# Kernel tuning notes

Hardware: AMD Instinct MI355X
Metric: run time of the kernel (lower is better)

Reference implementation:

```python
import jax, jax.numpy as jnp
import numpy as np

NUM_HEADS = 16


def rotary_pos_emb(x):
    # x: [b, h, s, d] with interleaved rotary pairs (d even)
    d, s = x.shape[-1], x.shape[-2]
    ts = jnp.arange(0, d, 2, dtype=jnp.float32)
    inv_freqs = 10000.0 ** (-ts / d)                      # [d/2]
    grid = jnp.arange(s, dtype=jnp.float32)[:, None] * inv_freqs[None, :]  # [s, d/2]
    sin = jnp.repeat(jnp.sin(grid), 2, axis=-1)           # [s, d]
    cos = jnp.repeat(jnp.cos(grid), 2, axis=-1)           # [s, d]
    x1, x2 = x[..., ::2], x[..., 1::2]
    xs = jnp.stack([-x2, x1], axis=-1).reshape(x.shape)   # rotate pairs
    return x * cos + xs * sin


def setup_inputs() -> dict:
    key = jax.random.key(0)
    ks = jax.random.split(key, 6)
    b, l, d = 2, 2048, 1024
    x = jax.random.normal(ks[0], (b, l, d), dtype=jnp.float32)
    # additive causal mask: 0 on/below diag, large negative above
    causal = jnp.tril(jnp.ones((l, l), dtype=bool))
    mask = jnp.where(causal, 0.0, -1e9).astype(jnp.float32)[None, None]  # [1,1,l,l]
    s = 0.01  # VarianceScaling(0.01)-ish small init
    Wq = jax.random.normal(ks[1], (d, d), dtype=jnp.float32) * s
    Wk = jax.random.normal(ks[2], (d, d), dtype=jnp.float32) * s
    Wv = jax.random.normal(ks[3], (d, d), dtype=jnp.float32) * s
    Wo = jax.random.normal(ks[4], (d, d), dtype=jnp.float32) * s
    return {"x": x, "mask": mask, "Wq": Wq, "Wk": Wk, "Wv": Wv, "Wo": Wo}


def reference(x, mask, Wq, Wk, Wv, Wo):
    b, l, d = x.shape
    h = NUM_HEADS
    k_sz = d // h
    split = lambda t: t.reshape(b, l, h, k_sz).transpose(0, 2, 1, 3)  # b h l k
    # NOTE: original scales q by 1/sqrt(model_dim) (not key_size), before RoPE
    q = split(x @ Wq / jnp.sqrt(jnp.float32(d)))
    q = rotary_pos_emb(q)
    k = rotary_pos_emb(split(x @ Wk))
    v = split(x @ Wv)
    logits = jnp.einsum('bhik,bhjk->bhij', q, k) + mask   # [b,h,l,l]
    a = jax.nn.softmax(logits, axis=-1)
    y = jnp.einsum('bhij,bhjv->bhiv', a, v)               # [b,h,l,k]
    y = y.transpose(0, 2, 1, 3).reshape(b, l, d)
    return y @ Wo
```

## Files before the change

kernel.cpp:

```cpp
#include <hip/hip_runtime.h>
#include <math.h>

#define L 2048
#define D 1024
#define H 16
#define KS 64
#define BBATCH 2

typedef float f32x4 __attribute__((ext_vector_type(4)));
typedef short s16x8 __attribute__((ext_vector_type(8)));

__device__ __forceinline__ ushort f2bf(float f) {
    union { float f; unsigned u; } v; v.f = f;
    unsigned lsb = (v.u >> 16) & 1u;
    v.u += 0x7fffu + lsb;
    return (ushort)(v.u >> 16);
}

__device__ __forceinline__ unsigned fbits(float f) {
    union { float f; unsigned u; } v; v.f = f; return v.u;
}

__device__ __forceinline__ void gl_lds16(const ushort* g, ushort* l) {
    __builtin_amdgcn_global_load_lds(
        (const __attribute__((address_space(1))) unsigned int*)g,
        (__attribute__((address_space(3))) unsigned int*)l, 16, 0, 0);
}

__global__ __launch_bounds__(256)
void conv_x(const float* __restrict__ x, ushort* __restrict__ xb)
{
    const int i = (blockIdx.x * 256 + threadIdx.x) * 4;
    const float4 v = *(const float4*)&x[i];
    ushort4 p = make_ushort4(f2bf(v.x), f2bf(v.y), f2bf(v.z), f2bf(v.w));
    *(ushort4*)&xb[i] = p;
}

__global__ __launch_bounds__(256)
void conv_w(const float* __restrict__ W0, const float* __restrict__ W1,
            const float* __restrict__ W2, const float* __restrict__ W3,
            ushort* __restrict__ Wt)
{
    const float* W = (blockIdx.z == 0) ? W0 : (blockIdx.z == 1) ? W1
                   : (blockIdx.z == 2) ? W2 : W3;
    ushort* out = Wt + (size_t)blockIdx.z * D * D;
    __shared__ float T[32][33];
    const int r0 = blockIdx.y * 32, c0 = blockIdx.x * 32;
    const int tr = threadIdx.x >> 3, tc = (threadIdx.x & 7) * 4;
    const float4 v = *(const float4*)&W[(size_t)(r0 + tr) * D + c0 + tc];
    T[tr][tc + 0] = v.x; T[tr][tc + 1] = v.y;
    T[tr][tc + 2] = v.z; T[tr][tc + 3] = v.w;
    __syncthreads();
    ushort4 p = make_ushort4(f2bf(T[tc + 0][tr]), f2bf(T[tc + 1][tr]),
                             f2bf(T[tc + 2][tr]), f2bf(T[tc + 3][tr]));
    *(ushort4*)&out[(size_t)(c0 + tr) * D + r0 + tc] = p;
}

__global__ __launch_bounds__(256)
void qkv_gemm(const ushort* __restrict__ A, const ushort* __restrict__ B,
              ushort* __restrict__ Qo, ushort* __restrict__ Ko,
              ushort* __restrict__ Vto)
{
    __shared__ __align__(16) ushort smem[18432];
    ushort* As = smem;
    ushort* Bs = smem + 4096;

    const int tid  = threadIdx.x;
    const int wv   = tid >> 6, lane = tid & 63;
    const int i16  = lane & 15, quad = lane >> 4;
    const int wr   = wv >> 1, wc = wv & 1;
    const int m0   = blockIdx.y * 128;
    const int n0   = blockIdx.x * 128;

    f32x4 acc[4][4];
    #pragma unroll
    for (int i = 0; i < 4; ++i)
        #pragma unroll
        for (int j = 0; j < 4; ++j) acc[i][j] = (f32x4){0.f, 0.f, 0.f, 0.f};

    for (int k0 = 0; k0 < D; k0 += 32) {
        __syncthreads();
        {
            int c = wv * 64 + lane;
            gl_lds16(A + (size_t)(m0 + (c >> 2)) * D + k0 + (c & 3) * 8,
                     As + (size_t)(wv * 64) * 8);
            c = 256 + wv * 64 + lane;
            gl_lds16(A + (size_t)(m0 + (c >> 2)) * D + k0 + (c & 3) * 8,
                     As + (size_t)(256 + wv * 64) * 8);
        }
        {
            int c = wv * 64 + lane;
            gl_lds16(B + (size_t)(n0 + (c >> 2)) * D + k0 + (c & 3) * 8,
                     Bs + (size_t)(wv * 64) * 8);
            c = 256 + wv * 64 + lane;
            gl_lds16(B + (size_t)(n0 + (c >> 2)) * D + k0 + (c & 3) * 8,
                     Bs + (size_t)(256 + wv * 64) * 8);
        }
        __syncthreads();
        s16x8 af[4], bf[4];
        #pragma unroll
        for (int mt = 0; mt < 4; ++mt)
            af[mt] = *(const s16x8*)&As[(wr * 64 + mt * 16 + i16) * 32 + quad * 8];
        #pragma unroll
        for (int nt = 0; nt < 4; ++nt)
            bf[nt] = *(const s16x8*)&Bs[(wc * 64 + nt * 16 + i16) * 32 + quad * 8];
        #pragma unroll
        for (int mt = 0; mt < 4; ++mt)
            #pragma unroll
            for (int nt = 0; nt < 4; ++nt)
                acc[mt][nt] = __builtin_amdgcn_mfma_f32_16x16x32_bf16(
                    af[mt], bf[nt], acc[mt][nt], 0, 0, 0);
    }

    if (m0 < 2048) {
        const bool isQ = (m0 < 1024);
        ushort* out = isQ ? Qo : Ko;
        const int mb = isQ ? m0 : (m0 - 1024);
        #pragma unroll
        for (int mt = 0; mt < 4; ++mt)
            #pragma unroll
            for (int nt = 0; nt < 4; ++nt) {
                const int token = n0 + wc * 64 + nt * 16 + i16;
                const int b = token >> 11, s = token & 2047;
                const int dim = mb + wr * 64 + mt * 16 + quad * 4;
                const int hh = dim >> 6, dd = dim & 63;
                const float sf = (float)s;
                ushort4 p;
                #pragma unroll
                for (int pr = 0; pr < 2; ++pr) {
                    float e = acc[mt][nt][2 * pr];
                    float o = acc[mt][nt][2 * pr + 1];
                    if (isQ) { e *= 0.03125f; o *= 0.03125f; }
                    const float inv = __expf(-(float)(dd + 2 * pr) *
                                             (9.210340371976184f / 64.0f));
                    const float ang = sf * inv;
                    float sn, cs;
                    sincosf(ang, &sn, &cs);
                    const float ne = e * cs - o * sn;
                    const float no = o * cs + e * sn;
                    if (pr == 0) { p.x = f2bf(ne); p.y = f2bf(no); }
                    else         { p.z = f2bf(ne); p.w = f2bf(no); }
                }
                *(ushort4*)&out[((size_t)(b * H + hh) * L + s) * KS + dd] = p;
            }
    } else {
        __syncthreads();
        ushort* T = smem + wv * 4608;
        const int vbase = (m0 - 2048) + wr * 64;
        const int tbase = n0 + wc * 64;
        #pragma unroll
        for (int mt = 0; mt < 4; ++mt)
            #pragma unroll
            for (int nt = 0; nt < 4; ++nt) {
                const int tl = nt * 16 + i16;
                #pragma unroll
                for (int r = 0; r < 4; ++r)
                    T[(mt * 16 + quad * 4 + r) * 72 + tl] = f2bf(acc[mt][nt][r]);
            }
        __builtin_amdgcn_s_waitcnt(0);
        const int tl0 = (lane & 7) * 8;
        #pragma unroll
        for (int c = 0; c < 8; ++c) {
            const int vl = c * 8 + (lane >> 3);
            const s16x8 val = *(const s16x8*)&T[vl * 72 + tl0];
            const int vdim = vbase + vl;
            const int hh = vdim >> 6, dd = vdim & 63;
            const int token0 = tbase + tl0;
            const int b = token0 >> 11, s0 = token0 & 2047;
            *(s16x8*)&Vto[((size_t)(b * H + hh) * KS + dd) * L + s0] = val;
        }
    }
}

__global__ __launch_bounds__(256)
void oproj_gemm(const ushort* __restrict__ A, const ushort* __restrict__ B,
                float* __restrict__ out)
{
    __shared__ __align__(16) ushort smem[8192];
    ushort* As = smem;
    ushort* Bs = smem + 4096;
    const int tid  = threadIdx.x;
    const int wv   = tid >> 6, lane = tid & 63;
    const int i16  = lane & 15, quad = lane >> 4;
    const int wr   = wv >> 1, wc = wv & 1;
    const int m0   = blockIdx.y * 128;
    const int n0   = blockIdx.x * 128;

    f32x4 acc[4][4];
    #pragma unroll
    for (int i = 0; i < 4; ++i)
        #pragma unroll
        for (int j = 0; j < 4; ++j) acc[i][j] = (f32x4){0.f, 0.f, 0.f, 0.f};

    for (int k0 = 0; k0 < D; k0 += 32) {
        __syncthreads();
        {
            int c = wv * 64 + lane;
            gl_lds16(A + (size_t)(m0 + (c >> 2)) * D + k0 + (c & 3) * 8,
                     As + (size_t)(wv * 64) * 8);
            c = 256 + wv * 64 + lane;
            gl_lds16(A + (size_t)(m0 + (c >> 2)) * D + k0 + (c & 3) * 8,
                     As + (size_t)(256 + wv * 64) * 8);
        }
        {
            int c = wv * 64 + lane;
            gl_lds16(B + (size_t)(n0 + (c >> 2)) * D + k0 + (c & 3) * 8,
                     Bs + (size_t)(wv * 64) * 8);
            c = 256 + wv * 64 + lane;
            gl_lds16(B + (size_t)(n0 + (c >> 2)) * D + k0 + (c & 3) * 8,
                     Bs + (size_t)(256 + wv * 64) * 8);
        }
        __syncthreads();
        s16x8 af[4], bf[4];
        #pragma unroll
        for (int mt = 0; mt < 4; ++mt)
            af[mt] = *(const s16x8*)&As[(wr * 64 + mt * 16 + i16) * 32 + quad * 8];
        #pragma unroll
        for (int nt = 0; nt < 4; ++nt)
            bf[nt] = *(const s16x8*)&Bs[(wc * 64 + nt * 16 + i16) * 32 + quad * 8];
        #pragma unroll
        for (int mt = 0; mt < 4; ++mt)
            #pragma unroll
            for (int nt = 0; nt < 4; ++nt)
                acc[mt][nt] = __builtin_amdgcn_mfma_f32_16x16x32_bf16(
                    af[mt], bf[nt], acc[mt][nt], 0, 0, 0);
    }

    #pragma unroll
    for (int mt = 0; mt < 4; ++mt)
        #pragma unroll
        for (int nt = 0; nt < 4; ++nt) {
            const int od = n0 + wc * 64 + nt * 16 + i16;
            const int tk = m0 + wr * 64 + mt * 16 + quad * 4;
            #pragma unroll
            for (int r = 0; r < 4; ++r)
                out[(size_t)(tk + r) * D + od] = acc[mt][nt][r];
        }
}

__global__ __launch_bounds__(512)
void attn_mfma(const ushort* __restrict__ Q, const ushort* __restrict__ K,
               const ushort* __restrict__ Vt, ushort* __restrict__ Yb)
{
    const int bh   = blockIdx.y;
    const int qa   = blockIdx.x;
    const int qb   = 31 - qa;
    const int tid  = threadIdx.x;
    const int wave = tid >> 6, lane = tid & 63;
    const int half = wave >> 2, wv4 = wave & 3;
    const int i16  = lane & 15, quad = lane >> 4;
    const int qt   = half ? qb : qa;
    const int r0   = qt * 64 + wv4 * 16;
    const int row  = r0 + i16;

    __shared__ ushort Ks[64 * 72];
    __shared__ ushort Vs[64 * 72];
    __shared__ ushort Ps[8][16 * 72];

    const ushort* Qb = Q  + (size_t)bh * L * KS;
    const ushort* Kb = K  + (size_t)bh * L * KS;
    const ushort* Vb = Vt + (size_t)bh * KS * L;

    const s16x8 qf0 = *(const s16x8*)(Qb + (size_t)row * KS + quad * 8);
    const s16x8 qf1 = *(const s16x8*)(Qb + (size_t)row * KS + 32 + quad * 8);

    const int sr = tid >> 3, sseg = (tid & 7) * 8;
    s16x8 kpre = *(const s16x8*)(Kb + (size_t)sr * KS + sseg);
    s16x8 vpre = *(const s16x8*)(Vb + (size_t)sr * L + sseg);
    *(s16x8*)&Ks[sr * 72 + sseg] = kpre;
    *(s16x8*)&Vs[sr * 72 + sseg] = vpre;
    __syncthreads();

    f32x4 O0 = {0.f,0.f,0.f,0.f}, O1 = O0, O2 = O0, O3 = O0;
    float psum = 0.0f;

    for (int jt = 0; jt <= qb; ++jt) {
        const int j0 = jt * 64;
        const bool has_next = (jt < qb);

        if (has_next) {
            const int j0n = j0 + 64;
            kpre = *(const s16x8*)(Kb + (size_t)(j0n + sr) * KS + sseg);
            vpre = *(const s16x8*)(Vb + (size_t)sr * L + j0n + sseg);
        }

        if (jt <= qt) {
            f32x4 st[4];
            #pragma unroll
            for (int nt = 0; nt < 4; ++nt) {
                const s16x8 kf0 = *(const s16x8*)&Ks[(nt * 16 + i16) * 72 + quad * 8];
                const s16x8 kf1 = *(const s16x8*)&Ks[(nt * 16 + i16) * 72 + 32 + quad * 8];
                f32x4 c = {0.f,0.f,0.f,0.f};
                c = __builtin_amdgcn_mfma_f32_16x16x32_bf16(kf0, qf0, c, 0, 0, 0);
                c = __builtin_amdgcn_mfma_f32_16x16x32_bf16(kf1, qf1, c, 0, 0, 0);
                st[nt] = c;
            }
            if (jt == qt) {
                #pragma unroll
                for (int nt = 0; nt < 4; ++nt)
                    #pragma unroll
                    for (int rg = 0; rg < 4; ++rg) {
                        const int j = j0 + nt * 16 + quad * 4 + rg;
                        if (j > row) st[nt][rg] = -1e30f;
                    }
            }
            float p[4][4];
            #pragma unroll
            for (int nt = 0; nt < 4; ++nt)
                #pragma unroll
                for (int rg = 0; rg < 4; ++rg) {
                    p[nt][rg] = __expf(st[nt][rg]);
                    psum += p[nt][rg];
                }
            ushort* P2 = &Ps[wave][0];
            #pragma unroll
            for (int nt = 0; nt < 4; ++nt) {
                uint2 pk;
                pk.x = __builtin_amdgcn_perm(fbits(p[nt][1]), fbits(p[nt][0]), 0x07060302u);
                pk.y = __builtin_amdgcn_perm(fbits(p[nt][3]), fbits(p[nt][2]), 0x07060302u);
                *(uint2*)(P2 + i16 * 72 + nt * 16 + quad * 4) = pk;
            }
            const s16x8 pf0 = *(const s16x8*)(P2 + i16 * 72 + quad * 8);
            const s16x8 pf1 = *(const s16x8*)(P2 + i16 * 72 + 32 + quad * 8);
            s16x8 v0, v1;
            v0 = *(const s16x8*)&Vs[(0 * 16 + i16) * 72 + quad * 8];
            v1 = *(const s16x8*)&Vs[(0 * 16 + i16) * 72 + 32 + quad * 8];
            O0 = __builtin_amdgcn_mfma_f32_16x16x32_bf16(v0, pf0, O0, 0, 0, 0);
            O0 = __builtin_amdgcn_mfma_f32_16x16x32_bf16(v1, pf1, O0, 0, 0, 0);
            v0 = *(const s16x8*)&Vs[(1 * 16 + i16) * 72 + quad * 8];
            v1 = *(const s16x8*)&Vs[(1 * 16 + i16) * 72 + 32 + quad * 8];
            O1 = __builtin_amdgcn_mfma_f32_16x16x32_bf16(v0, pf0, O1, 0, 0, 0);
            O1 = __builtin_amdgcn_mfma_f32_16x16x32_bf16(v1, pf1, O1, 0, 0, 0);
            v0 = *(const s16x8*)&Vs[(2 * 16 + i16) * 72 + quad * 8];
            v1 = *(const s16x8*)&Vs[(2 * 16 + i16) * 72 + 32 + quad * 8];
            O2 = __builtin_amdgcn_mfma_f32_16x16x32_bf16(v0, pf0, O2, 0, 0, 0);
            O2 = __builtin_amdgcn_mfma_f32_16x16x32_bf16(v1, pf1, O2, 0, 0, 0);
            v0 = *(const s16x8*)&Vs[(3 * 16 + i16) * 72 + quad * 8];
            v1 = *(const s16x8*)&Vs[(3 * 16 + i16) * 72 + 32 + quad * 8];
            O3 = __builtin_amdgcn_mfma_f32_16x16x32_bf16(v0, pf0, O3, 0, 0, 0);
            O3 = __builtin_amdgcn_mfma_f32_16x16x32_bf16(v1, pf1, O3, 0, 0, 0);
        }

        __syncthreads();
        if (has_next) {
            *(s16x8*)&Ks[sr * 72 + sseg] = kpre;
            *(s16x8*)&Vs[sr * 72 + sseg] = vpre;
        }
        __syncthreads();
    }

    psum += __shfl_xor(psum, 16);
    psum += __shfl_xor(psum, 32);
    const float inv_l = __builtin_amdgcn_rcpf(psum);
    const int b = bh >> 4, hh = bh & 15;
    ushort* Yp = Yb + ((size_t)(b * L + row)) * D + hh * KS + quad * 4;
    f32x4 r;
    r = O0 * inv_l; *(ushort4*)(Yp +  0) = make_ushort4(f2bf(r[0]),f2bf(r[1]),f2bf(r[2]),f2bf(r[3]));
    r = O1 * inv_l; *(ushort4*)(Yp + 16) = make_ushort4(f2bf(r[0]),f2bf(r[1]),f2bf(r[2]),f2bf(r[3]));
    r = O2 * inv_l; *(ushort4*)(Yp + 32) = make_ushort4(f2bf(r[0]),f2bf(r[1]),f2bf(r[2]),f2bf(r[3]));
    r = O3 * inv_l; *(ushort4*)(Yp + 48) = make_ushort4(f2bf(r[0]),f2bf(r[1]),f2bf(r[2]),f2bf(r[3]));
}

extern "C" void kernel_launch(void* const* d_in, const int* in_sizes, int n_in,
                              void* d_out, int out_size, void* d_ws, size_t ws_size,
                              hipStream_t stream)
{
    const float* x  = (const float*)d_in[0];
    const float* Wq = (const float*)d_in[2];
    const float* Wk = (const float*)d_in[3];
    const float* Wv = (const float*)d_in[4];
    const float* Wo = (const float*)d_in[5];

    const size_t NTOK = (size_t)BBATCH * L;
    const size_t SZ   = NTOK * D;
    ushort* xb  = (ushort*)d_ws;
    ushort* Wt  = xb + SZ;
    ushort* Qb  = Wt + 4 * (size_t)D * D;
    ushort* Kb  = Qb + SZ;
    ushort* Vtb = Kb + SZ;
    ushort* Yb  = Vtb + SZ;

    conv_x<<<dim3(SZ / 1024), dim3(256), 0, stream>>>(x, xb);
    conv_w<<<dim3(32, 32, 4), dim3(256), 0, stream>>>(Wq, Wk, Wv, Wo, Wt);

    qkv_gemm<<<dim3(32, 24), dim3(256), 0, stream>>>(Wt, xb, Qb, Kb, Vtb);

    attn_mfma<<<dim3(16, 32), dim3(512), 0, stream>>>(Qb, Kb, Vtb, Yb);

    oproj_gemm<<<dim3(8, 32), dim3(256), 0, stream>>>(Yb, Wt + 3 * (size_t)D * D,
                                                      (float*)d_out);
}
```

Measured before the change: 197.6 us.

## Fuse prep kernels, precompute RoPE table, split attention KV across waves, shrink oproj tiles

Merges the x and weight conversion kernels into one prep launch that also builds a cos/sin table for RoPE, which the QKV GEMM epilogue reads instead of calling sincosf per element. The attention kernel changes from pairing two query tiles per block to one query tile per block, with two wave groups each taking alternate KV tiles and merging partial outputs and sums through shared memory at the end. The output-projection GEMM uses 128x64 tiles for twice as many blocks. The cost is an extra table read and LDS reduction, and the table lives in the Yb buffer before attention overwrites it.

```diff
diff --git a/kernel.cpp b/kernel.cpp
--- a/kernel.cpp
+++ b/kernel.cpp
@@ -28,36 +28,47 @@
 }
 
 __global__ __launch_bounds__(256)
-void conv_x(const float* __restrict__ x, ushort* __restrict__ xb)
+void prep(const float* __restrict__ x,
+          const float* __restrict__ W0, const float* __restrict__ W1,
+          const float* __restrict__ W2, const float* __restrict__ W3,
+          ushort* __restrict__ xb, ushort* __restrict__ Wt,
+          float2* __restrict__ tab)
 {
-    const int i = (blockIdx.x * 256 + threadIdx.x) * 4;
-    const float4 v = *(const float4*)&x[i];
-    ushort4 p = make_ushort4(f2bf(v.x), f2bf(v.y), f2bf(v.z), f2bf(v.w));
-    *(ushort4*)&xb[i] = p;
-}
-
-__global__ __launch_bounds__(256)
-void conv_w(const float* __restrict__ W0, const float* __restrict__ W1,
-            const float* __restrict__ W2, const float* __restrict__ W3,
-            ushort* __restrict__ Wt)
-{
-    const float* W = (blockIdx.z == 0) ? W0 : (blockIdx.z == 1) ? W1
-                   : (blockIdx.z == 2) ? W2 : W3;
-    ushort* out = Wt + (size_t)blockIdx.z * D * D;
     __shared__ float T[32][33];
-    const int r0 = blockIdx.y * 32, c0 = blockIdx.x * 32;
-    const int tr = threadIdx.x >> 3, tc = (threadIdx.x & 7) * 4;
-    const float4 v = *(const float4*)&W[(size_t)(r0 + tr) * D + c0 + tc];
-    T[tr][tc + 0] = v.x; T[tr][tc + 1] = v.y;
-    T[tr][tc + 2] = v.z; T[tr][tc + 3] = v.w;
-    __syncthreads();
-    ushort4 p = make_ushort4(f2bf(T[tc + 0][tr]), f2bf(T[tc + 1][tr]),
-                             f2bf(T[tc + 2][tr]), f2bf(T[tc + 3][tr]));
-    *(ushort4*)&out[(size_t)(c0 + tr) * D + r0 + tc] = p;
+    const int bid = blockIdx.x;
+    const int tid = threadIdx.x;
+    if (bid < 4096) {
+        const int i = bid * 1024 + tid * 4;
+        const float4 v = *(const float4*)&x[i];
+        ushort4 p = make_ushort4(f2bf(v.x), f2bf(v.y), f2bf(v.z), f2bf(v.w));
+        *(ushort4*)&xb[i] = p;
+    } else if (bid < 8192) {
+        const int t = bid - 4096;
+        const int z = t >> 10;
+        const float* W = (z == 0) ? W0 : (z == 1) ? W1 : (z == 2) ? W2 : W3;
+        ushort* out = Wt + (size_t)z * D * D;
+        const int r0 = ((t >> 5) & 31) * 32, c0 = (t & 31) * 32;
+        const int tr = tid >> 3, tc = (tid & 7) * 4;
+        const float4 v = *(const float4*)&W[(size_t)(r0 + tr) * D + c0 + tc];
+        T[tr][tc + 0] = v.x; T[tr][tc + 1] = v.y;
+        T[tr][tc + 2] = v.z; T[tr][tc + 3] = v.w;
+        __syncthreads();
+        ushort4 p = make_ushort4(f2bf(T[tc + 0][tr]), f2bf(T[tc + 1][tr]),
+                                 f2bf(T[tc + 2][tr]), f2bf(T[tc + 3][tr]));
+        *(ushort4*)&out[(size_t)(c0 + tr) * D + r0 + tc] = p;
+    } else {
+        const int idx = (bid - 8192) * 256 + tid;
+        const int dd2 = idx >> 11, s = idx & 2047;
+        const float inv = __expf(-(float)(2 * dd2) * (9.210340371976184f / 64.0f));
+        float sn, cs;
+        sincosf((float)s * inv, &sn, &cs);
+        tab[idx] = make_float2(cs, sn);
+    }
 }
 
 __global__ __launch_bounds__(256)
 void qkv_gemm(const ushort* __restrict__ A, const ushort* __restrict__ B,
+              const float2* __restrict__ tab,
               ushort* __restrict__ Qo, ushort* __restrict__ Ko,
               ushort* __restrict__ Vto)
 {
@@ -124,20 +135,15 @@
                 const int b = token >> 11, s = token & 2047;
                 const int dim = mb + wr * 64 + mt * 16 + quad * 4;
                 const int hh = dim >> 6, dd = dim & 63;
-                const float sf = (float)s;
                 ushort4 p;
                 #pragma unroll
                 for (int pr = 0; pr < 2; ++pr) {
                     float e = acc[mt][nt][2 * pr];
                     float o = acc[mt][nt][2 * pr + 1];
                     if (isQ) { e *= 0.03125f; o *= 0.03125f; }
-                    const float inv = __expf(-(float)(dd + 2 * pr) *
-                                             (9.210340371976184f / 64.0f));
-                    const float ang = sf * inv;
-                    float sn, cs;
-                    sincosf(ang, &sn, &cs);
-                    const float ne = e * cs - o * sn;
-                    const float no = o * cs + e * sn;
+                    const float2 cssn = tab[(size_t)((dd >> 1) + pr) * 2048 + s];
+                    const float ne = e * cssn.x - o * cssn.y;
+                    const float no = o * cssn.x + e * cssn.y;
                     if (pr == 0) { p.x = f2bf(ne); p.y = f2bf(no); }
                     else         { p.z = f2bf(ne); p.w = f2bf(no); }
                 }
@@ -176,21 +182,20 @@
 void oproj_gemm(const ushort* __restrict__ A, const ushort* __restrict__ B,
                 float* __restrict__ out)
 {
-    __shared__ __align__(16) ushort smem[8192];
-    ushort* As = smem;
-    ushort* Bs = smem + 4096;
+    __shared__ __align__(16) ushort As[128 * 32];
+    __shared__ __align__(16) ushort Bs[64 * 32];
     const int tid  = threadIdx.x;
     const int wv   = tid >> 6, lane = tid & 63;
     const int i16  = lane & 15, quad = lane >> 4;
     const int wr   = wv >> 1, wc = wv & 1;
     const int m0   = blockIdx.y * 128;
-    const int n0   = blockIdx.x * 128;
-
-    f32x4 acc[4][4];
+    const int n0   = blockIdx.x * 64;
+
+    f32x4 acc[4][2];
     #pragma unroll
     for (int i = 0; i < 4; ++i)
         #pragma unroll
-        for (int j = 0; j < 4; ++j) acc[i][j] = (f32x4){0.f, 0.f, 0.f, 0.f};
+        for (int j = 0; j < 2; ++j) acc[i][j] = (f32x4){0.f, 0.f, 0.f, 0.f};
 
     for (int k0 = 0; k0 < D; k0 += 32) {
         __syncthreads();
@@ -206,22 +211,19 @@
             int c = wv * 64 + lane;
             gl_lds16(B + (size_t)(n0 + (c >> 2)) * D + k0 + (c & 3) * 8,
                      Bs + (size_t)(wv * 64) * 8);
-            c = 256 + wv * 64 + lane;
-            gl_lds16(B + (size_t)(n0 + (c >> 2)) * D + k0 + (c & 3) * 8,
-                     Bs + (size_t)(256 + wv * 64) * 8);
-        }
-        __syncthreads();
-        s16x8 af[4], bf[4];
+        }
+        __syncthreads();
+        s16x8 af[4], bf[2];
         #pragma unroll
         for (int mt = 0; mt < 4; ++mt)
             af[mt] = *(const s16x8*)&As[(wr * 64 + mt * 16 + i16) * 32 + quad * 8];
         #pragma unroll
-        for (int nt = 0; nt < 4; ++nt)
-            bf[nt] = *(const s16x8*)&Bs[(wc * 64 + nt * 16 + i16) * 32 + quad * 8];
-        #pragma unroll
-        for (int mt = 0; mt < 4; ++mt)
-            #pragma unroll
-            for (int nt = 0; nt < 4; ++nt)
+        for (int nt = 0; nt < 2; ++nt)
+            bf[nt] = *(const s16x8*)&Bs[(wc * 32 + nt * 16 + i16) * 32 + quad * 8];
+        #pragma unroll
+        for (int mt = 0; mt < 4; ++mt)
+            #pragma unroll
+            for (int nt = 0; nt < 2; ++nt)
                 acc[mt][nt] = __builtin_amdgcn_mfma_f32_16x16x32_bf16(
                     af[mt], bf[nt], acc[mt][nt], 0, 0, 0);
     }
@@ -229,8 +231,8 @@
     #pragma unroll
     for (int mt = 0; mt < 4; ++mt)
         #pragma unroll
-        for (int nt = 0; nt < 4; ++nt) {
-            const int od = n0 + wc * 64 + nt * 16 + i16;
+        for (int nt = 0; nt < 2; ++nt) {
+            const int od = n0 + wc * 32 + nt * 16 + i16;
             const int tk = m0 + wr * 64 + mt * 16 + quad * 4;
             #pragma unroll
             for (int r = 0; r < 4; ++r)
@@ -243,19 +245,15 @@
                const ushort* __restrict__ Vt, ushort* __restrict__ Yb)
 {
     const int bh   = blockIdx.y;
-    const int qa   = blockIdx.x;
-    const int qb   = 31 - qa;
+    const int qt   = 31 - blockIdx.x;
     const int tid  = threadIdx.x;
     const int wave = tid >> 6, lane = tid & 63;
-    const int half = wave >> 2, wv4 = wave & 3;
+    const int qs   = wave & 3, par = wave >> 2;
     const int i16  = lane & 15, quad = lane >> 4;
-    const int qt   = half ? qb : qa;
-    const int r0   = qt * 64 + wv4 * 16;
-    const int row  = r0 + i16;
-
-    __shared__ ushort Ks[64 * 72];
-    __shared__ ushort Vs[64 * 72];
-    __shared__ ushort Ps[8][16 * 72];
+    const int row  = qt * 64 + qs * 16 + i16;
+
+    __shared__ __align__(16) ushort KVs[4][64 * 72];
+    __shared__ __align__(16) ushort Ps[8][16 * 72];
 
     const ushort* Qb = Q  + (size_t)bh * L * KS;
     const ushort* Kb = K  + (size_t)bh * L * KS;
@@ -264,38 +262,57 @@
     const s16x8 qf0 = *(const s16x8*)(Qb + (size_t)row * KS + quad * 8);
     const s16x8 qf1 = *(const s16x8*)(Qb + (size_t)row * KS + 32 + quad * 8);
 
-    const int sr = tid >> 3, sseg = (tid & 7) * 8;
-    s16x8 kpre = *(const s16x8*)(Kb + (size_t)sr * KS + sseg);
-    s16x8 vpre = *(const s16x8*)(Vb + (size_t)sr * L + sseg);
-    *(s16x8*)&Ks[sr * 72 + sseg] = kpre;
-    *(s16x8*)&Vs[sr * 72 + sseg] = vpre;
+    const int sr = tid >> 3, ss = (tid & 7) * 8;
+
+    s16x8 kpA, vpA, kpB, vpB;
+    kpA = *(const s16x8*)(Kb + (size_t)sr * KS + ss);
+    vpA = *(const s16x8*)(Vb + (size_t)sr * L + ss);
+    if (qt >= 1) {
+        kpB = *(const s16x8*)(Kb + (size_t)(64 + sr) * KS + ss);
+        vpB = *(const s16x8*)(Vb + (size_t)sr * L + 64 + ss);
+    }
+    *(s16x8*)&KVs[0][sr * 72 + ss] = kpA;
+    *(s16x8*)&KVs[1][sr * 72 + ss] = vpA;
+    if (qt >= 1) {
+        *(s16x8*)&KVs[2][sr * 72 + ss] = kpB;
+        *(s16x8*)&KVs[3][sr * 72 + ss] = vpB;
+    }
     __syncthreads();
 
     f32x4 O0 = {0.f,0.f,0.f,0.f}, O1 = O0, O2 = O0, O3 = O0;
     float psum = 0.0f;
 
-    for (int jt = 0; jt <= qb; ++jt) {
-        const int j0 = jt * 64;
-        const bool has_next = (jt < qb);
-
-        if (has_next) {
-            const int j0n = j0 + 64;
-            kpre = *(const s16x8*)(Kb + (size_t)(j0n + sr) * KS + sseg);
-            vpre = *(const s16x8*)(Vb + (size_t)sr * L + j0n + sseg);
-        }
-
-        if (jt <= qt) {
+    const ushort* Ksb = &KVs[par * 2][0];
+    const ushort* Vsb = &KVs[par * 2 + 1][0];
+    ushort* P2 = &Ps[wave][0];
+
+    for (int p = 0; ; ++p) {
+        const int jme = 2 * p + par;
+        const bool pn = (2 * p + 2 <= qt);
+
+        if (pn) {
+            const int ja = (2 * p + 2) * 64;
+            kpA = *(const s16x8*)(Kb + (size_t)(ja + sr) * KS + ss);
+            vpA = *(const s16x8*)(Vb + (size_t)sr * L + ja + ss);
+            if (2 * p + 3 <= qt) {
+                kpB = *(const s16x8*)(Kb + (size_t)(ja + 64 + sr) * KS + ss);
+                vpB = *(const s16x8*)(Vb + (size_t)sr * L + ja + 64 + ss);
+            }
+        }
+
+        if (jme <= qt) {
+            const int j0 = jme * 64;
             f32x4 st[4];
             #pragma unroll
             for (int nt = 0; nt < 4; ++nt) {
-                const s16x8 kf0 = *(const s16x8*)&Ks[(nt * 16 + i16) * 72 + quad * 8];
-                const s16x8 kf1 = *(const s16x8*)&Ks[(nt * 16 + i16) * 72 + 32 + quad * 8];
+                const s16x8 kf0 = *(const s16x8*)&Ksb[(nt * 16 + i16) * 72 + quad * 8];
+                const s16x8 kf1 = *(const s16x8*)&Ksb[(nt * 16 + i16) * 72 + 32 + quad * 8];
                 f32x4 c = {0.f,0.f,0.f,0.f};
                 c = __builtin_amdgcn_mfma_f32_16x16x32_bf16(kf0, qf0, c, 0, 0, 0);
                 c = __builtin_amdgcn_mfma_f32_16x16x32_bf16(kf1, qf1, c, 0, 0, 0);
                 st[nt] = c;
             }
-            if (jt == qt) {
+            if (jme == qt) {
                 #pragma unroll
                 for (int nt = 0; nt < 4; ++nt)
                     #pragma unroll
@@ -304,61 +321,85 @@
                         if (j > row) st[nt][rg] = -1e30f;
                     }
             }
-            float p[4][4];
+            float pv[4][4];
             #pragma unroll
             for (int nt = 0; nt < 4; ++nt)
                 #pragma unroll
                 for (int rg = 0; rg < 4; ++rg) {
-                    p[nt][rg] = __expf(st[nt][rg]);
-                    psum += p[nt][rg];
+                    pv[nt][rg] = __expf(st[nt][rg]);
+                    psum += pv[nt][rg];
                 }
-            ushort* P2 = &Ps[wave][0];
             #pragma unroll
             for (int nt = 0; nt < 4; ++nt) {
                 uint2 pk;
-                pk.x = __builtin_amdgcn_perm(fbits(p[nt][1]), fbits(p[nt][0]), 0x07060302u);
-                pk.y = __builtin_amdgcn_perm(fbits(p[nt][3]), fbits(p[nt][2]), 0x07060302u);
+                pk.x = __builtin_amdgcn_perm(fbits(pv[nt][1]), fbits(pv[nt][0]), 0x07060302u);
+                pk.y = __builtin_amdgcn_perm(fbits(pv[nt][3]), fbits(pv[nt][2]), 0x07060302u);
                 *(uint2*)(P2 + i16 * 72 + nt * 16 + quad * 4) = pk;
             }
             const s16x8 pf0 = *(const s16x8*)(P2 + i16 * 72 + quad * 8);
             const s16x8 pf1 = *(const s16x8*)(P2 + i16 * 72 + 32 + quad * 8);
             s16x8 v0, v1;
-            v0 = *(const s16x8*)&Vs[(0 * 16 + i16) * 72 + quad * 8];
-            v1 = *(const s16x8*)&Vs[(0 * 16 + i16) * 72 + 32 + quad * 8];
+            v0 = *(const s16x8*)&Vsb[(0 * 16 + i16) * 72 + quad * 8];
+            v1 = *(const s16x8*)&Vsb[(0 * 16 + i16) * 72 + 32 + quad * 8];
             O0 = __builtin_amdgcn_mfma_f32_16x16x32_bf16(v0, pf0, O0, 0, 0, 0);
             O0 = __builtin_amdgcn_mfma_f32_16x16x32_bf16(v1, pf1, O0, 0, 0, 0);
-            v0 = *(const s16x8*)&Vs[(1 * 16 + i16) * 72 + quad * 8];
-            v1 = *(const s16x8*)&Vs[(1 * 16 + i16) * 72 + 32 + quad * 8];
+            v0 = *(const s16x8*)&Vsb[(1 * 16 + i16) * 72 + quad * 8];
+            v1 = *(const s16x8*)&Vsb[(1 * 16 + i16) * 72 + 32 + quad * 8];
             O1 = __builtin_amdgcn_mfma_f32_16x16x32_bf16(v0, pf0, O1, 0, 0, 0);
             O1 = __builtin_amdgcn_mfma_f32_16x16x32_bf16(v1, pf1, O1, 0, 0, 0);
-            v0 = *(const s16x8*)&Vs[(2 * 16 + i16) * 72 + quad * 8];
-            v1 = *(const s16x8*)&Vs[(2 * 16 + i16) * 72 + 32 + quad * 8];
+            v0 = *(const s16x8*)&Vsb[(2 * 16 + i16) * 72 + quad * 8];
+            v1 = *(const s16x8*)&Vsb[(2 * 16 + i16) * 72 + 32 + quad * 8];
             O2 = __builtin_amdgcn_mfma_f32_16x16x32_bf16(v0, pf0, O2, 0, 0, 0);
             O2 = __builtin_amdgcn_mfma_f32_16x16x32_bf16(v1, pf1, O2, 0, 0, 0);
-            v0 = *(const s16x8*)&Vs[(3 * 16 + i16) * 72 + quad * 8];
-            v1 = *(const s16x8*)&Vs[(3 * 16 + i16) * 72 + 32 + quad * 8];
+            v0 = *(const s16x8*)&Vsb[(3 * 16 + i16) * 72 + quad * 8];
+            v1 = *(const s16x8*)&Vsb[(3 * 16 + i16) * 72 + 32 + quad * 8];
             O3 = __builtin_amdgcn_mfma_f32_16x16x32_bf16(v0, pf0, O3, 0, 0, 0);
             O3 = __builtin_amdgcn_mfma_f32_16x16x32_bf16(v1, pf1, O3, 0, 0, 0);
         }
 
-        __syncthreads();
-        if (has_next) {
-            *(s16x8*)&Ks[sr * 72 + sseg] = kpre;
-            *(s16x8*)&Vs[sr * 72 + sseg] = vpre;
+        if (!pn) break;
+        __syncthreads();
+        {
+            *(s16x8*)&KVs[0][sr * 72 + ss] = kpA;
+            *(s16x8*)&KVs[1][sr * 72 + ss] = vpA;
+            if (2 * p + 3 <= qt) {
+                *(s16x8*)&KVs[2][sr * 72 + ss] = kpB;
+                *(s16x8*)&KVs[3][sr * 72 + ss] = vpB;
+            }
         }
         __syncthreads();
     }
 
     psum += __shfl_xor(psum, 16);
     psum += __shfl_xor(psum, 32);
-    const float inv_l = __builtin_amdgcn_rcpf(psum);
-    const int b = bh >> 4, hh = bh & 15;
-    ushort* Yp = Yb + ((size_t)(b * L + row)) * D + hh * KS + quad * 4;
-    f32x4 r;
-    r = O0 * inv_l; *(ushort4*)(Yp +  0) = make_ushort4(f2bf(r[0]),f2bf(r[1]),f2bf(r[2]),f2bf(r[3]));
-    r = O1 * inv_l; *(ushort4*)(Yp + 16) = make_ushort4(f2bf(r[0]),f2bf(r[1]),f2bf(r[2]),f2bf(r[3]));
-    r = O2 * inv_l; *(ushort4*)(Yp + 32) = make_ushort4(f2bf(r[0]),f2bf(r[1]),f2bf(r[2]),f2bf(r[3]));
-    r = O3 * inv_l; *(ushort4*)(Yp + 48) = make_ushort4(f2bf(r[0]),f2bf(r[1]),f2bf(r[2]),f2bf(r[3]));
+
+    __syncthreads();
+    float* Oex = (float*)&KVs[0][0];
+    float* Pex = Oex + 64 * 68;
+    const int obase = (qs * 16 + i16) * 68 + quad * 4;
+    if (par == 1) {
+        *(f32x4*)&Oex[obase +  0] = O0;
+        *(f32x4*)&Oex[obase + 16] = O1;
+        *(f32x4*)&Oex[obase + 32] = O2;
+        *(f32x4*)&Oex[obase + 48] = O3;
+        if (lane < 16) Pex[qs * 16 + i16] = psum;
+    }
+    __syncthreads();
+    if (par == 0) {
+        O0 += *(const f32x4*)&Oex[obase +  0];
+        O1 += *(const f32x4*)&Oex[obase + 16];
+        O2 += *(const f32x4*)&Oex[obase + 32];
+        O3 += *(const f32x4*)&Oex[obase + 48];
+        const float tot = psum + Pex[qs * 16 + i16];
+        const float inv_l = __builtin_amdgcn_rcpf(tot);
+        const int b = bh >> 4, hh = bh & 15;
+        ushort* Yp = Yb + ((size_t)(b * L + row)) * D + hh * KS + quad * 4;
+        f32x4 r;
+        r = O0 * inv_l; *(ushort4*)(Yp +  0) = make_ushort4(f2bf(r[0]),f2bf(r[1]),f2bf(r[2]),f2bf(r[3]));
+        r = O1 * inv_l; *(ushort4*)(Yp + 16) = make_ushort4(f2bf(r[0]),f2bf(r[1]),f2bf(r[2]),f2bf(r[3]));
+        r = O2 * inv_l; *(ushort4*)(Yp + 32) = make_ushort4(f2bf(r[0]),f2bf(r[1]),f2bf(r[2]),f2bf(r[3]));
+        r = O3 * inv_l; *(ushort4*)(Yp + 48) = make_ushort4(f2bf(r[0]),f2bf(r[1]),f2bf(r[2]),f2bf(r[3]));
+    }
 }
 
 extern "C" void kernel_launch(void* const* d_in, const int* in_sizes, int n_in,
@@ -379,14 +420,14 @@
     ushort* Kb  = Qb + SZ;
     ushort* Vtb = Kb + SZ;
     ushort* Yb  = Vtb + SZ;
-
-    conv_x<<<dim3(SZ / 1024), dim3(256), 0, stream>>>(x, xb);
-    conv_w<<<dim3(32, 32, 4), dim3(256), 0, stream>>>(Wq, Wk, Wv, Wo, Wt);
-
-    qkv_gemm<<<dim3(32, 24), dim3(256), 0, stream>>>(Wt, xb, Qb, Kb, Vtb);
-
-    attn_mfma<<<dim3(16, 32), dim3(512), 0, stream>>>(Qb, Kb, Vtb, Yb);
-
-    oproj_gemm<<<dim3(8, 32), dim3(256), 0, stream>>>(Yb, Wt + 3 * (size_t)D * D,
-                                                      (float*)d_out);
-}
+    float2* tab = (float2*)Yb;
+
+    prep<<<dim3(8448), dim3(256), 0, stream>>>(x, Wq, Wk, Wv, Wo, xb, Wt, tab);
+
+    qkv_gemm<<<dim3(32, 24), dim3(256), 0, stream>>>(Wt, xb, tab, Qb, Kb, Vtb);
+
+    attn_mfma<<<dim3(32, 32), dim3(512), 0, stream>>>(Qb, Kb, Vtb, Yb);
+
+    oproj_gemm<<<dim3(16, 32), dim3(256), 0, stream>>>(Yb, Wt + 3 * (size_t)D * D,
+                                                       (float*)d_out);
+}
```

After: 219.8 us. 11.2% more time.

## Merge prep kernels, tabulate RoPE sin/cos, stage Q/K stores via LDS, shrink oproj tile

Applied to the files above, without the earlier changes.

Fuses the x and weight bf16 conversion kernels into one prep launch, which also builds a precomputed cos/sin table for RoPE in the Y workspace buffer. The QKV GEMM epilogue reads that table instead of calling expf and sincosf per element, and stages rotated Q/K tiles in LDS so global stores become coalesced 16-byte rows. The output projection uses 128x64 tiles to double the block count for better CU occupancy. The table lookups add global reads, and reusing the Y buffer for the table relies on attention overwriting it afterwards.

```diff
diff --git a/kernel.cpp b/kernel.cpp
--- a/kernel.cpp
+++ b/kernel.cpp
@@ -28,36 +28,47 @@
 }
 
 __global__ __launch_bounds__(256)
-void conv_x(const float* __restrict__ x, ushort* __restrict__ xb)
+void prep(const float* __restrict__ x,
+          const float* __restrict__ W0, const float* __restrict__ W1,
+          const float* __restrict__ W2, const float* __restrict__ W3,
+          ushort* __restrict__ xb, ushort* __restrict__ Wt,
+          float2* __restrict__ tab)
 {
-    const int i = (blockIdx.x * 256 + threadIdx.x) * 4;
-    const float4 v = *(const float4*)&x[i];
-    ushort4 p = make_ushort4(f2bf(v.x), f2bf(v.y), f2bf(v.z), f2bf(v.w));
-    *(ushort4*)&xb[i] = p;
-}
-
-__global__ __launch_bounds__(256)
-void conv_w(const float* __restrict__ W0, const float* __restrict__ W1,
-            const float* __restrict__ W2, const float* __restrict__ W3,
-            ushort* __restrict__ Wt)
-{
-    const float* W = (blockIdx.z == 0) ? W0 : (blockIdx.z == 1) ? W1
-                   : (blockIdx.z == 2) ? W2 : W3;
-    ushort* out = Wt + (size_t)blockIdx.z * D * D;
     __shared__ float T[32][33];
-    const int r0 = blockIdx.y * 32, c0 = blockIdx.x * 32;
-    const int tr = threadIdx.x >> 3, tc = (threadIdx.x & 7) * 4;
-    const float4 v = *(const float4*)&W[(size_t)(r0 + tr) * D + c0 + tc];
-    T[tr][tc + 0] = v.x; T[tr][tc + 1] = v.y;
-    T[tr][tc + 2] = v.z; T[tr][tc + 3] = v.w;
-    __syncthreads();
-    ushort4 p = make_ushort4(f2bf(T[tc + 0][tr]), f2bf(T[tc + 1][tr]),
-                             f2bf(T[tc + 2][tr]), f2bf(T[tc + 3][tr]));
-    *(ushort4*)&out[(size_t)(c0 + tr) * D + r0 + tc] = p;
+    const int bid = blockIdx.x;
+    const int tid = threadIdx.x;
+    if (bid < 4096) {
+        const int i = bid * 1024 + tid * 4;
+        const float4 v = *(const float4*)&x[i];
+        ushort4 p = make_ushort4(f2bf(v.x), f2bf(v.y), f2bf(v.z), f2bf(v.w));
+        *(ushort4*)&xb[i] = p;
+    } else if (bid < 8192) {
+        const int t = bid - 4096;
+        const int z = t >> 10;
+        const float* W = (z == 0) ? W0 : (z == 1) ? W1 : (z == 2) ? W2 : W3;
+        ushort* out = Wt + (size_t)z * D * D;
+        const int r0 = ((t >> 5) & 31) * 32, c0 = (t & 31) * 32;
+        const int tr = tid >> 3, tc = (tid & 7) * 4;
+        const float4 v = *(const float4*)&W[(size_t)(r0 + tr) * D + c0 + tc];
+        T[tr][tc + 0] = v.x; T[tr][tc + 1] = v.y;
+        T[tr][tc + 2] = v.z; T[tr][tc + 3] = v.w;
+        __syncthreads();
+        ushort4 p = make_ushort4(f2bf(T[tc + 0][tr]), f2bf(T[tc + 1][tr]),
+                                 f2bf(T[tc + 2][tr]), f2bf(T[tc + 3][tr]));
+        *(ushort4*)&out[(size_t)(c0 + tr) * D + r0 + tc] = p;
+    } else {
+        const int idx = (bid - 8192) * 256 + tid;
+        const int dd2 = idx >> 11, s = idx & 2047;
+        const float inv = __expf(-(float)(2 * dd2) * (9.210340371976184f / 64.0f));
+        float sn, cs;
+        sincosf((float)s * inv, &sn, &cs);
+        tab[idx] = make_float2(cs, sn);
+    }
 }
 
 __global__ __launch_bounds__(256)
 void qkv_gemm(const ushort* __restrict__ A, const ushort* __restrict__ B,
+              const float2* __restrict__ tab,
               ushort* __restrict__ Qo, ushort* __restrict__ Ko,
               ushort* __restrict__ Vto)
 {
@@ -112,40 +123,48 @@
                     af[mt], bf[nt], acc[mt][nt], 0, 0, 0);
     }
 
+    __syncthreads();
+    ushort* T = smem + wv * 4608;
+
     if (m0 < 2048) {
         const bool isQ = (m0 < 1024);
         ushort* out = isQ ? Qo : Ko;
         const int mb = isQ ? m0 : (m0 - 1024);
-        #pragma unroll
-        for (int mt = 0; mt < 4; ++mt)
+        const int s0 = ((n0 + wc * 64) & 2047);
+        #pragma unroll
+        for (int mt = 0; mt < 4; ++mt) {
+            const int dd = mt * 16 + quad * 4;
             #pragma unroll
             for (int nt = 0; nt < 4; ++nt) {
-                const int token = n0 + wc * 64 + nt * 16 + i16;
-                const int b = token >> 11, s = token & 2047;
-                const int dim = mb + wr * 64 + mt * 16 + quad * 4;
-                const int hh = dim >> 6, dd = dim & 63;
-                const float sf = (float)s;
+                const int lt = nt * 16 + i16;
+                const int s = s0 + lt;
                 ushort4 p;
                 #pragma unroll
                 for (int pr = 0; pr < 2; ++pr) {
                     float e = acc[mt][nt][2 * pr];
                     float o = acc[mt][nt][2 * pr + 1];
                     if (isQ) { e *= 0.03125f; o *= 0.03125f; }
-                    const float inv = __expf(-(float)(dd + 2 * pr) *
-                                             (9.210340371976184f / 64.0f));
-                    const float ang = sf * inv;
-                    float sn, cs;
-                    sincosf(ang, &sn, &cs);
-                    const float ne = e * cs - o * sn;
-                    const float no = o * cs + e * sn;
+                    const float2 cssn = tab[(size_t)((dd >> 1) + pr) * 2048 + s];
+                    const float ne = e * cssn.x - o * cssn.y;
+                    const float no = o * cssn.x + e * cssn.y;
                     if (pr == 0) { p.x = f2bf(ne); p.y = f2bf(no); }
                     else         { p.z = f2bf(ne); p.w = f2bf(no); }
                 }
-                *(ushort4*)&out[((size_t)(b * H + hh) * L + s) * KS + dd] = p;
+                *(ushort4*)&T[lt * 72 + dd] = p;
             }
+        }
+        __builtin_amdgcn_s_waitcnt(0);
+        const int hh = (mb + wr * 64) >> 6;
+        const int tok0 = n0 + wc * 64;
+        const int b = tok0 >> 11;
+        const int dl = (lane & 7) * 8;
+        #pragma unroll
+        for (int c = 0; c < 8; ++c) {
+            const int tl = c * 8 + (lane >> 3);
+            const s16x8 val = *(const s16x8*)&T[tl * 72 + dl];
+            *(s16x8*)&out[((size_t)(b * H + hh) * L + (s0 + tl)) * KS + dl] = val;
+        }
     } else {
-        __syncthreads();
-        ushort* T = smem + wv * 4608;
         const int vbase = (m0 - 2048) + wr * 64;
         const int tbase = n0 + wc * 64;
         #pragma unroll
@@ -166,8 +185,8 @@
             const int vdim = vbase + vl;
             const int hh = vdim >> 6, dd = vdim & 63;
             const int token0 = tbase + tl0;
-            const int b = token0 >> 11, s0 = token0 & 2047;
-            *(s16x8*)&Vto[((size_t)(b * H + hh) * KS + dd) * L + s0] = val;
+            const int b = token0 >> 11, sv = token0 & 2047;
+            *(s16x8*)&Vto[((size_t)(b * H + hh) * KS + dd) * L + sv] = val;
         }
     }
 }
@@ -176,21 +195,20 @@
 void oproj_gemm(const ushort* __restrict__ A, const ushort* __restrict__ B,
                 float* __restrict__ out)
 {
-    __shared__ __align__(16) ushort smem[8192];
-    ushort* As = smem;
-    ushort* Bs = smem + 4096;
+    __shared__ __align__(16) ushort As[128 * 32];
+    __shared__ __align__(16) ushort Bs[64 * 32];
     const int tid  = threadIdx.x;
     const int wv   = tid >> 6, lane = tid & 63;
     const int i16  = lane & 15, quad = lane >> 4;
     const int wr   = wv >> 1, wc = wv & 1;
     const int m0   = blockIdx.y * 128;
-    const int n0   = blockIdx.x * 128;
-
-    f32x4 acc[4][4];
+    const int n0   = blockIdx.x * 64;
+
+    f32x4 acc[4][2];
     #pragma unroll
     for (int i = 0; i < 4; ++i)
         #pragma unroll
-        for (int j = 0; j < 4; ++j) acc[i][j] = (f32x4){0.f, 0.f, 0.f, 0.f};
+        for (int j = 0; j < 2; ++j) acc[i][j] = (f32x4){0.f, 0.f, 0.f, 0.f};
 
     for (int k0 = 0; k0 < D; k0 += 32) {
         __syncthreads();
@@ -206,22 +224,19 @@
             int c = wv * 64 + lane;
             gl_lds16(B + (size_t)(n0 + (c >> 2)) * D + k0 + (c & 3) * 8,
                      Bs + (size_t)(wv * 64) * 8);
-            c = 256 + wv * 64 + lane;
-            gl_lds16(B + (size_t)(n0 + (c >> 2)) * D + k0 + (c & 3) * 8,
-                     Bs + (size_t)(256 + wv * 64) * 8);
-        }
-        __syncthreads();
-        s16x8 af[4], bf[4];
+        }
+        __syncthreads();
+        s16x8 af[4], bf[2];
         #pragma unroll
         for (int mt = 0; mt < 4; ++mt)
             af[mt] = *(const s16x8*)&As[(wr * 64 + mt * 16 + i16) * 32 + quad * 8];
         #pragma unroll
-        for (int nt = 0; nt < 4; ++nt)
-            bf[nt] = *(const s16x8*)&Bs[(wc * 64 + nt * 16 + i16) * 32 + quad * 8];
+        for (int nt = 0; nt < 2; ++nt)
+            bf[nt] = *(const s16x8*)&Bs[(wc * 32 + nt * 16 + i16) * 32 + quad * 8];
         #pragma unroll
         for (int mt = 0; mt < 4; ++mt)
             #pragma unroll
-            for (int nt = 0; nt < 4; ++nt)
+            for (int nt = 0; nt < 2; ++nt)
                 acc[mt][nt] = __builtin_amdgcn_mfma_f32_16x16x32_bf16(
                     af[mt], bf[nt], acc[mt][nt], 0, 0, 0);
     }
@@ -229,8 +244,8 @@
     #pragma unroll
     for (int mt = 0; mt < 4; ++mt)
         #pragma unroll
-        for (int nt = 0; nt < 4; ++nt) {
-            const int od = n0 + wc * 64 + nt * 16 + i16;
+        for (int nt = 0; nt < 2; ++nt) {
+            const int od = n0 + wc * 32 + nt * 16 + i16;
             const int tk = m0 + wr * 64 + mt * 16 + quad * 4;
             #pragma unroll
             for (int r = 0; r < 4; ++r)
@@ -304,20 +319,20 @@
                         if (j > row) st[nt][rg] = -1e30f;
                     }
             }
-            float p[4][4];
+            float pv[4][4];
             #pragma unroll
             for (int nt = 0; nt < 4; ++nt)
                 #pragma unroll
                 for (int rg = 0; rg < 4; ++rg) {
-                    p[nt][rg] = __expf(st[nt][rg]);
-                    psum += p[nt][rg];
+                    pv[nt][rg] = __expf(st[nt][rg]);
+                    psum += pv[nt][rg];
                 }
             ushort* P2 = &Ps[wave][0];
             #pragma unroll
             for (int nt = 0; nt < 4; ++nt) {
                 uint2 pk;
-                pk.x = __builtin_amdgcn_perm(fbits(p[nt][1]), fbits(p[nt][0]), 0x07060302u);
-                pk.y = __builtin_amdgcn_perm(fbits(p[nt][3]), fbits(p[nt][2]), 0x07060302u);
+                pk.x = __builtin_amdgcn_perm(fbits(pv[nt][1]), fbits(pv[nt][0]), 0x07060302u);
+                pk.y = __builtin_amdgcn_perm(fbits(pv[nt][3]), fbits(pv[nt][2]), 0x07060302u);
                 *(uint2*)(P2 + i16 * 72 + nt * 16 + quad * 4) = pk;
             }
             const s16x8 pf0 = *(const s16x8*)(P2 + i16 * 72 + quad * 8);
@@ -379,14 +394,14 @@
     ushort* Kb  = Qb + SZ;
     ushort* Vtb = Kb + SZ;
     ushort* Yb  = Vtb + SZ;
-
-    conv_x<<<dim3(SZ / 1024), dim3(256), 0, stream>>>(x, xb);
-    conv_w<<<dim3(32, 32, 4), dim3(256), 0, stream>>>(Wq, Wk, Wv, Wo, Wt);
-
-    qkv_gemm<<<dim3(32, 24), dim3(256), 0, stream>>>(Wt, xb, Qb, Kb, Vtb);
+    float2* tab = (float2*)Yb;
+
+    prep<<<dim3(8448), dim3(256), 0, stream>>>(x, Wq, Wk, Wv, Wo, xb, Wt, tab);
+
+    qkv_gemm<<<dim3(32, 24), dim3(256), 0, stream>>>(Wt, xb, tab, Qb, Kb, Vtb);
 
     attn_mfma<<<dim3(16, 32), dim3(512), 0, stream>>>(Qb, Kb, Vtb, Yb);
 
-    oproj_gemm<<<dim3(8, 32), dim3(256), 0, stream>>>(Yb, Wt + 3 * (size_t)D * D,
-                                                      (float*)d_out);
-}
+    oproj_gemm<<<dim3(16, 32), dim3(256), 0, stream>>>(Yb, Wt + 3 * (size_t)D * D,
+                                                       (float*)d_out);
+}
```

Result: no change. 200.7 us (+1.6%).
